# Performance work log

Measured on AMD Instinct MI355X. Metric: run time of the kernel, lower is better.

Reference implementation:

```python
import jax, jax.numpy as jnp
import numpy as np

B, L, D, H, K = 4, 2048, 1024, 16, 256
DH = D // H
SCALE = DH ** -0.5


def setup_inputs() -> dict:
    key = jax.random.key(0)
    ks = jax.random.split(key, 8)
    std = 1.0 / np.sqrt(D)
    pstd = 1.0 / np.sqrt(K)  # init_ uses last dim of (seq_len, k) tensor
    return {
        "x": jax.random.normal(ks[0], (B, L, D), dtype=jnp.float32),
        "Wq": jax.random.uniform(ks[1], (D, D), jnp.float32, -std, std),
        "Wk": jax.random.uniform(ks[2], (D, D), jnp.float32, -std, std),
        "Wv": jax.random.uniform(ks[3], (D, D), jnp.float32, -std, std),
        "proj_k": jax.random.uniform(ks[4], (L, K), jnp.float32, -pstd, pstd),
        "proj_v": jax.random.uniform(ks[5], (L, K), jnp.float32, -pstd, pstd),
        "Wo": jax.random.uniform(ks[6], (D, D), jnp.float32, -std, std),
        "bo": jax.random.uniform(ks[7], (D,), jnp.float32, -std, std),
    }


def reference(x, Wq, Wk, Wv, proj_k, proj_v, Wo, bo):
    b, l, d = x.shape
    q = x @ Wq.T                                   # [B,L,D]
    keys = jnp.einsum("bnd,nk->bkd", x @ Wk.T, proj_k)   # [B,K,D]
    vals = jnp.einsum("bnd,nk->bkd", x @ Wv.T, proj_v)   # [B,K,D]
    # faithful to original: plain reshape (B,h,L,d_h), NOT transpose-split
    q = q.reshape(b, H, l, DH)
    k = keys.reshape(b, K, H, DH).transpose(0, 2, 1, 3)  # [B,H,K,DH]
    v = vals.reshape(b, K, H, DH).transpose(0, 2, 1, 3)  # [B,H,K,DH]
    attn = jax.nn.softmax(jnp.einsum("bhld,bhkd->bhlk", q, k) * SCALE, axis=-1)
    out = jnp.einsum("bhlk,bhkd->bhld", attn, v)
    out = out.transpose(0, 2, 1, 3).reshape(b, l, d)
    return out @ Wo.T + bo
```

## Files before the change

kernel.cpp:

```cpp
#include <hip/hip_runtime.h>


typedef __attribute__((ext_vector_type(8))) short short8;
typedef __attribute__((ext_vector_type(4))) short short4_t;
typedef __attribute__((ext_vector_type(4))) float facc;

#define B_    4
#define L_    2048
#define D_    1024
#define H_    16
#define KP    256
#define DH_   64
#define SCALE_ 0.125f
#define PTS   76

__device__ __forceinline__ short f2b(float f) {
  unsigned u = __float_as_uint(f);
  unsigned r = (u + 0x7fffu + ((u >> 16) & 1u)) >> 16;
  return (short)r;
}

__device__ __forceinline__ void load16_to_lds(const short* gp, short* lp) {
  __builtin_amdgcn_global_load_lds(
      (const __attribute__((address_space(1))) void*)gp,
      (__attribute__((address_space(3))) void*)lp, 16, 0, 0);
}

__global__ __launch_bounds__(256) void prepX(
    const float* __restrict__ x,  const float* __restrict__ pk,
    const float* __restrict__ pv, const float* __restrict__ w0,
    const float* __restrict__ w1, const float* __restrict__ w2,
    const float* __restrict__ w3, short* __restrict__ xb,
    short* __restrict__ xTb, short* __restrict__ projT,
    short* __restrict__ Wb)
{
  const int z = blockIdx.z, tid = threadIdx.x;
  if (z >= 6) {
    const int bid  = blockIdx.y * 32 + blockIdx.x;
    const int widx = (z - 6) * 2 + (bid >> 10);
    const float* s = (widx == 0) ? w0 : (widx == 1) ? w1 : (widx == 2) ? w2 : w3;
    const int i = ((bid & 1023) * 256 + tid) * 4;
    float4 f = *(const float4*)(s + i);
    short4_t v; v[0] = f2b(f.x); v[1] = f2b(f.y); v[2] = f2b(f.z); v[3] = f2b(f.w);
    *(short4_t*)(Wb + (size_t)widx * 1048576 + i) = v;
    return;
  }

  __shared__ float tl[32][37];
  const int row = tid >> 3, c4 = tid & 7;

  if (z < 4) {
    const int b = z, l0 = blockIdx.y * 32, d0 = blockIdx.x * 32;
    const float* s = x + (size_t)b * L_ * D_;
    float4 f = *(const float4*)(s + (size_t)(l0 + row) * D_ + d0 + c4 * 4);
    short4_t v; v[0] = f2b(f.x); v[1] = f2b(f.y); v[2] = f2b(f.z); v[3] = f2b(f.w);
    *(short4_t*)(xb + (size_t)b * L_ * D_ + (size_t)(l0 + row) * D_ + d0 + c4 * 4) = v;
    tl[row][c4 * 4 + 0] = f.x; tl[row][c4 * 4 + 1] = f.y;
    tl[row][c4 * 4 + 2] = f.z; tl[row][c4 * 4 + 3] = f.w;
    __syncthreads();
    short4_t t;
#pragma unroll
    for (int j = 0; j < 4; j++) t[j] = f2b(tl[c4 * 4 + j][row]);
    *(short4_t*)(xTb + (size_t)b * D_ * L_ + (size_t)(d0 + row) * L_ + l0 + c4 * 4) = t;
  } else {
    if (blockIdx.x >= 8) return;
    const int sel = z - 4, l0 = blockIdx.y * 32, k0 = blockIdx.x * 32;
    const float* s = sel ? pv : pk;
    float4 f = *(const float4*)(s + (size_t)(l0 + row) * KP + k0 + c4 * 4);
    tl[row][c4 * 4 + 0] = f.x; tl[row][c4 * 4 + 1] = f.y;
    tl[row][c4 * 4 + 2] = f.z; tl[row][c4 * 4 + 3] = f.w;
    __syncthreads();
    short4_t t;
#pragma unroll
    for (int j = 0; j < 4; j++) t[j] = f2b(tl[c4 * 4 + j][row]);
    *(short4_t*)(projT + (size_t)sel * (KP * L_) + (size_t)(k0 + row) * L_ + l0 + c4 * 4) = t;
  }
}

__global__ __launch_bounds__(512, 2) void gemm8p(
    const short* __restrict__ Am, const short* __restrict__ Bm,
    const float* __restrict__ bias, float* __restrict__ C32,
    short* __restrict__ Cb, int M, int N, int K)
{
  extern __shared__ __attribute__((aligned(16))) short smem[];
  constexpr int BUF  = 24576;
  constexpr int BOFF = 16384;

  const int t = threadIdx.x, lane = t & 63, w = t >> 6;
  const int lm = lane & 15, g = lane >> 4;
  const int bm = blockIdx.x * 4 + (blockIdx.y >> 3);
  const int bn = blockIdx.y & 7;
  const int m0 = bm * 256, n0 = bn * 128;
  const int wm = (w & 3) * 64, wn = (w >> 2) * 64;

  const int srow = lane >> 2;
  const int sslot = lane & 3;

  facc acc[4][4];
  const facc fz = {0.f, 0.f, 0.f, 0.f};
#pragma unroll
  for (int i = 0; i < 4; i++)
#pragma unroll
    for (int j = 0; j < 4; j++) acc[i][j] = fz;

  auto stageA = [&](int kt, int buf, int rnd) {
    const int task = rnd * 8 + w;
    const int c = task >> 4, grp = task & 15;
    const int row = grp * 16 + srow;
    const int slot = sslot ^ ((row >> 1) & 3);
    load16_to_lds(Am + (size_t)(m0 + row) * K + kt * 64 + c * 32 + slot * 8,
                  smem + buf * BUF + c * 8192 + grp * 512);
  };
  auto stageB = [&](int kt, int buf, int rnd) {
    const int task = rnd * 8 + w;
    const int c = task >> 3, grp = task & 7;
    const int row = grp * 16 + srow;
    const int slot = sslot ^ ((row >> 1) & 3);
    load16_to_lds(Bm + (size_t)(n0 + row) * K + kt * 64 + c * 32 + slot * 8,
                  smem + buf * BUF + BOFF + c * 4096 + grp * 512);
  };

#pragma unroll
  for (int r = 0; r < 4; r++) stageA(0, 0, r);
#pragma unroll
  for (int r = 0; r < 2; r++) stageB(0, 0, r);
#pragma unroll
  for (int r = 0; r < 4; r++) stageA(1, 1, r);
#pragma unroll
  for (int r = 0; r < 2; r++) stageB(1, 1, r);
  asm volatile("s_waitcnt vmcnt(6)" ::: "memory");
  __builtin_amdgcn_sched_barrier(0);
  __builtin_amdgcn_s_barrier();

  const int T = K >> 6;
  int p = 0;
  for (int kt = 0; kt < T; kt++) {
    const int q = (p == 0) ? 2 : p - 1;
    const bool pf = (kt + 2 < T);

#pragma unroll
    for (int c = 0; c < 2; c++) {
      short8 af[4], bf[4];
      const int abase = p * BUF + c * 8192;
      const int bbase = p * BUF + BOFF + c * 4096;
#pragma unroll
      for (int mt = 0; mt < 4; mt++) {
        const int row = wm + 16 * mt + lm;
        af[mt] = *(const short8*)(smem + abase + row * 32 + ((g ^ ((row >> 1) & 3)) * 8));
      }
#pragma unroll
      for (int nt = 0; nt < 4; nt++) {
        const int row = wn + 16 * nt + lm;
        bf[nt] = *(const short8*)(smem + bbase + row * 32 + ((g ^ ((row >> 1) & 3)) * 8));
      }
      if (pf) {
        if (c == 0) { stageA(kt + 2, q, 0); stageA(kt + 2, q, 1); stageB(kt + 2, q, 0); }
        else        { stageA(kt + 2, q, 2); stageA(kt + 2, q, 3); stageB(kt + 2, q, 1); }
      }
      __builtin_amdgcn_s_barrier();
      __builtin_amdgcn_s_setprio(1);
#pragma unroll
      for (int mt = 0; mt < 4; mt++)
#pragma unroll
        for (int nt = 0; nt < 4; nt++)
          acc[mt][nt] = __builtin_amdgcn_mfma_f32_16x16x32_bf16(af[mt], bf[nt], acc[mt][nt], 0, 0, 0);
      __builtin_amdgcn_s_setprio(0);
      if (c == 0) __builtin_amdgcn_s_barrier();
    }

    if (pf) {
      asm volatile("s_waitcnt vmcnt(6)" ::: "memory");
      __builtin_amdgcn_sched_barrier(0);
    } else if (kt + 1 < T) {
      asm volatile("s_waitcnt vmcnt(0)" ::: "memory");
      __builtin_amdgcn_sched_barrier(0);
    }
    __builtin_amdgcn_s_barrier();
    p = (p == 2) ? 0 : p + 1;
  }

#pragma unroll
  for (int mt = 0; mt < 4; mt++)
#pragma unroll
    for (int r = 0; r < 4; r++) {
      const int row = m0 + wm + 16 * mt + 4 * g + r;
#pragma unroll
      for (int nt = 0; nt < 4; nt++) {
        const int col = n0 + wn + 16 * nt + lm;
        float v = acc[mt][nt][r];
        if (bias) v += bias[col];
        if (C32) C32[(size_t)row * N + col] = v;
        if (Cb)  Cb[(size_t)row * N + col] = f2b(v);
      }
    }
}

__global__ __launch_bounds__(256) void gemm_p64(
    const short* __restrict__ Am, const short* __restrict__ Bm,
    const float* __restrict__ bias, float* __restrict__ C32,
    short* __restrict__ Cb, short* __restrict__ CbT, int M, int N, int K,
    long aHi, long aLo, long bHi, long bLo, long cHi, long cLo, int zDiv)
{
  __shared__ __attribute__((aligned(16))) short smem[3 * 8192];
  const int t = threadIdx.x, lane = t & 63, w = t >> 6;
  const int lm = lane & 15, g = lane >> 4;
  const int z = blockIdx.z, zhi = z / zDiv, zlo = z % zDiv;
  const int bm = blockIdx.y, bn = blockIdx.x;
  const int m0 = bm * 64, n0 = bn * 64;
  const int wm = (w & 1) * 32, wn = (w >> 1) * 32;

  const short* Ab = Am + zhi * aHi + zlo * aLo;
  const short* Bp = Bm + zhi * bHi + zlo * bLo;

  const int srow = w * 16 + (lane >> 2);
  const int pslot = (lane & 3) ^ ((srow >> 1) & 3);

  facc acc[2][2];
  const facc fz = {0.f, 0.f, 0.f, 0.f};
#pragma unroll
  for (int i = 0; i < 2; i++)
#pragma unroll
    for (int j = 0; j < 2; j++) acc[i][j] = fz;

  auto stage_h = [&](int kt, int buf, int c) {
    load16_to_lds(Ab + (size_t)(m0 + srow) * K + kt * 64 + c * 32 + pslot * 8,
                  smem + buf * 8192 + c * 2048 + w * 512);
    load16_to_lds(Bp + (size_t)(n0 + srow) * K + kt * 64 + c * 32 + pslot * 8,
                  smem + buf * 8192 + 4096 + c * 2048 + w * 512);
  };

  stage_h(0, 0, 0); stage_h(0, 0, 1);
  stage_h(1, 1, 0); stage_h(1, 1, 1);
  asm volatile("s_waitcnt vmcnt(4)" ::: "memory");
  __builtin_amdgcn_sched_barrier(0);
  __builtin_amdgcn_s_barrier();

  const int T = K >> 6;
  int p = 0;
  for (int kt = 0; kt < T; kt++) {
    const int q = (p == 0) ? 2 : p - 1;
    const bool pf = (kt + 2 < T);

#pragma unroll
    for (int c = 0; c < 2; c++) {
      short8 af[2], bf[2];
      const int abase = p * 8192 + c * 2048;
      const int bbase = p * 8192 + 4096 + c * 2048;
#pragma unroll
      for (int mt = 0; mt < 2; mt++) {
        const int row = wm + 16 * mt + lm;
        af[mt] = *(const short8*)(smem + abase + row * 32 + ((g ^ ((row >> 1) & 3)) * 8));
      }
#pragma unroll
      for (int nt = 0; nt < 2; nt++) {
        const int row = wn + 16 * nt + lm;
        bf[nt] = *(const short8*)(smem + bbase + row * 32 + ((g ^ ((row >> 1) & 3)) * 8));
      }
      if (pf) stage_h(kt + 2, q, c);
      __builtin_amdgcn_s_setprio(1);
#pragma unroll
      for (int mt = 0; mt < 2; mt++)
#pragma unroll
        for (int nt = 0; nt < 2; nt++)
          acc[mt][nt] = __builtin_amdgcn_mfma_f32_16x16x32_bf16(af[mt], bf[nt], acc[mt][nt], 0, 0, 0);
      __builtin_amdgcn_s_setprio(0);
    }

    if (pf) {
      asm volatile("s_waitcnt vmcnt(4)" ::: "memory");
      __builtin_amdgcn_sched_barrier(0);
    } else if (kt + 1 < T) {
      asm volatile("s_waitcnt vmcnt(0)" ::: "memory");
      __builtin_amdgcn_sched_barrier(0);
    }
    __builtin_amdgcn_s_barrier();
    p = (p == 2) ? 0 : p + 1;
  }

  if (CbT && zhi == 1) {
#pragma unroll
    for (int mt = 0; mt < 2; mt++) {
      const int rb = m0 + wm + 16 * mt + 4 * g;
      const size_t bb = (size_t)(rb >> 8) * (16 * 64 * 256);
      const int kp = rb & 255;
#pragma unroll
      for (int nt = 0; nt < 2; nt++) {
        const int col = n0 + wn + 16 * nt + lm;
        short4_t o4;
#pragma unroll
        for (int r = 0; r < 4; r++) o4[r] = f2b(acc[mt][nt][r]);
        *(short4_t*)(CbT + bb + (size_t)col * KP + kp) = o4;
      }
    }
    return;
  }

  const long cz = zhi * cHi + zlo * cLo;
#pragma unroll
  for (int mt = 0; mt < 2; mt++)
#pragma unroll
    for (int r = 0; r < 4; r++) {
      const int row = m0 + wm + 16 * mt + 4 * g + r;
#pragma unroll
      for (int nt = 0; nt < 2; nt++) {
        const int col = n0 + wn + 16 * nt + lm;
        float v = acc[mt][nt][r];
        if (bias) v += bias[col];
        if (C32) C32[cz + (size_t)row * N + col] = v;
        if (Cb)  Cb[cz + (size_t)row * N + col] = f2b(v);
      }
    }
}

__global__ __launch_bounds__(256) void attn_mfma(
    const short* __restrict__ xqb, const short* __restrict__ keysb,
    const short* __restrict__ vTb, short* __restrict__ out2b)
{
  __shared__ __attribute__((aligned(16))) short Kt[2][64 * 72];
  __shared__ __attribute__((aligned(16))) short Vt[2][64 * 72];
  __shared__ __attribute__((aligned(16))) short Pt[4][32 * PTS];

  const int t = threadIdx.x, lane = t & 63, w = t >> 6;
  const int lm = lane & 15, g = lane >> 4;
  const int b = blockIdx.z, h = blockIdx.y;
  const int l0w = blockIdx.x * 128 + w * 32;

  short8 aq[2][2];
#pragma unroll
  for (int mt = 0; mt < 2; mt++) {
    const int l = l0w + 16 * mt + lm;
    const short* qrow = xqb + ((size_t)b * L_ + h * 128 + (l >> 4)) * D_ + (l & 15) * DH_;
#pragma unroll
    for (int ks = 0; ks < 2; ks++)
      aq[mt][ks] = *(const short8*)(qrow + ks * 32 + g * 8);
  }

  facc accO[2][4];
  const facc fz = {0.f, 0.f, 0.f, 0.f};
#pragma unroll
  for (int mt = 0; mt < 2; mt++)
#pragma unroll
    for (int dt = 0; dt < 4; dt++) accO[mt][dt] = fz;
  float lrow[2][4];
#pragma unroll
  for (int mt = 0; mt < 2; mt++)
#pragma unroll
    for (int r = 0; r < 4; r++) lrow[mt][r] = 0.f;

  const short* Kb = keysb + (size_t)b * KP * D_ + h * DH_;
  const short* Vb = vTb + ((size_t)b * H_ + h) * DH_ * KP;

  const int srow = t >> 3, sch = (t & 7) * 8;

#pragma unroll
  for (int i = 0; i < 2; i++) {
    const int row = srow + 32 * i;
    *(short8*)(&Kt[0][row * 72 + sch]) = *(const short8*)(Kb + (size_t)row * D_ + sch);
    *(short8*)(&Vt[0][row * 72 + sch]) = *(const short8*)(Vb + (size_t)row * KP + sch);
  }
  __syncthreads();

  for (int c = 0; c < 4; c++) {
    const int bi = c & 1;

    short8 kr[2], vr[2];
    if (c < 3) {
#pragma unroll
      for (int i = 0; i < 2; i++) {
        const int row = srow + 32 * i;
        kr[i] = *(const short8*)(Kb + (size_t)((c + 1) * 64 + row) * D_ + sch);
        vr[i] = *(const short8*)(Vb + (size_t)row * KP + (c + 1) * 64 + sch);
      }
    }

    facc S[2][4];
#pragma unroll
    for (int mt = 0; mt < 2; mt++)
#pragma unroll
      for (int nt = 0; nt < 4; nt++) S[mt][nt] = fz;
#pragma unroll
    for (int ks = 0; ks < 2; ks++) {
      short8 bk[4];
#pragma unroll
      for (int nt = 0; nt < 4; nt++)
        bk[nt] = *(const short8*)(&Kt[bi][(16 * nt + lm) * 72 + ks * 32 + g * 8]);
#pragma unroll
      for (int mt = 0; mt < 2; mt++)
#pragma unroll
        for (int nt = 0; nt < 4; nt++)
          S[mt][nt] = __builtin_amdgcn_mfma_f32_16x16x32_bf16(aq[mt][ks], bk[nt], S[mt][nt], 0, 0, 0);
    }

    if (c < 3) {
#pragma unroll
      for (int i = 0; i < 2; i++) {
        const int row = srow + 32 * i;
        *(short8*)(&Kt[bi ^ 1][row * 72 + sch]) = kr[i];
        *(short8*)(&Vt[bi ^ 1][row * 72 + sch]) = vr[i];
      }
    }

#pragma unroll
    for (int mt = 0; mt < 2; mt++)
#pragma unroll
      for (int r = 0; r < 4; r++) {
        float ps = 0.f;
        const int prow = (16 * mt + 4 * g + r) * PTS;
#pragma unroll
        for (int nt = 0; nt < 4; nt++) {
          const float p = __expf(S[mt][nt][r] * SCALE_);
          ps += p;
          Pt[w][prow + 16 * nt + lm] = f2b(p);
        }
        lrow[mt][r] += ps;
      }

#pragma unroll
    for (int ks = 0; ks < 2; ks++) {
      short8 ap[2], bv[4];
#pragma unroll
      for (int mt = 0; mt < 2; mt++)
        ap[mt] = *(const short8*)(&Pt[w][(16 * mt + lm) * PTS + ks * 32 + g * 8]);
#pragma unroll
      for (int dt = 0; dt < 4; dt++)
        bv[dt] = *(const short8*)(&Vt[bi][(16 * dt + lm) * 72 + ks * 32 + g * 8]);
#pragma unroll
      for (int mt = 0; mt < 2; mt++)
#pragma unroll
        for (int dt = 0; dt < 4; dt++)
          accO[mt][dt] = __builtin_amdgcn_mfma_f32_16x16x32_bf16(ap[mt], bv[dt], accO[mt][dt], 0, 0, 0);
    }
    __syncthreads();
  }

#pragma unroll
  for (int mt = 0; mt < 2; mt++)
#pragma unroll
    for (int r = 0; r < 4; r++) {
      float ls = lrow[mt][r];
      ls += __shfl_xor(ls, 1);
      ls += __shfl_xor(ls, 2);
      ls += __shfl_xor(ls, 4);
      ls += __shfl_xor(ls, 8);
      const float inv = 1.0f / ls;
      const int l = l0w + 16 * mt + 4 * g + r;
#pragma unroll
      for (int dt = 0; dt < 4; dt++)
        out2b[((size_t)b * L_ + l) * D_ + h * DH_ + 16 * dt + lm] = f2b(accO[mt][dt][r] * inv);
    }
}

extern "C" void kernel_launch(void* const* d_in, const int* in_sizes, int n_in,
                              void* d_out, int out_size, void* d_ws, size_t ws_size,
                              hipStream_t stream)
{
  const float* x      = (const float*)d_in[0];
  const float* Wq     = (const float*)d_in[1];
  const float* Wk     = (const float*)d_in[2];
  const float* Wv     = (const float*)d_in[3];
  const float* proj_k = (const float*)d_in[4];
  const float* proj_v = (const float*)d_in[5];
  const float* Wo     = (const float*)d_in[6];
  const float* bo     = (const float*)d_in[7];
  float* out = (float*)d_out;

  short* ws     = (short*)d_ws;
  short* xqb    = ws;
  short* xTb    = xqb    + 8388608;
  short* xb     = xTb    + 8388608;
  short* out2b  = xb;
  short* Wqb    = xb     + 8388608;
  short* Wkb    = Wqb    + 1048576;
  short* Wvb    = Wkb    + 1048576;
  short* Wob    = Wvb    + 1048576;
  short* projTk = Wob    + 1048576;
  short* projTv = projTk + 524288;
  short* xk2b   = projTv + 524288;
  short* xv2b   = xk2b   + 1048576;
  short* keysb  = xv2b   + 1048576;
  short* valsb  = keysb  + 1048576;
  short* vT     = valsb  + 1048576;
  (void)Wkb; (void)Wvb; (void)projTv; (void)xv2b; (void)valsb;

  static bool attr_set = false;
  if (!attr_set) {
    (void)hipFuncSetAttribute(reinterpret_cast<const void*>(gemm8p),
                              hipFuncAttributeMaxDynamicSharedMemorySize, 147456);
    attr_set = true;
  }

  prepX<<<dim3(32, 64, 8), 256, 0, stream>>>(
      x, proj_k, proj_v, Wq, Wk, Wv, Wo, xb, xTb, projTk, Wqb);

  gemm8p<<<dim3(8, 32, 1), 512, 147456, stream>>>(
      xb, Wqb, nullptr, nullptr, xqb, 8192, 1024, 1024);

  gemm_p64<<<dim3(16, 4, 8), 256, 0, stream>>>(
      projTk, xTb, nullptr, nullptr, xk2b, nullptr, 256, 1024, 2048,
      524288, 0, 0, (long)D_ * L_, 1048576, 262144, 4);

  gemm_p64<<<dim3(16, 16, 2), 256, 0, stream>>>(
      xk2b, Wkb, nullptr, nullptr, keysb, vT, 1024, 1024, 1024,
      1048576, 0, 1048576, 0, 0, 0, 1);

  attn_mfma<<<dim3(16, 16, 4), 256, 0, stream>>>(xqb, keysb, vT, out2b);

  gemm8p<<<dim3(8, 32, 1), 512, 147456, stream>>>(
      out2b, Wob, bo, out, nullptr, 8192, 1024, 1024);
}
```

Before: 216.0 us.

## Widen projection GEMM tile to 64x128 and read K/V directly in attention

The small projection GEMM kernel now computes a 64x128 output tile per block instead of 64x64. Each wave owns 32x64 of it, B staging loads double and the LDS ring grows, which is meant to raise MFMA work per A fetch and halve the grid. Separately, the attention kernel drops its double-buffered LDS staging of K and V and the per-chunk __syncthreads, and loads MFMA operands straight from global memory. That removes barriers and LDS traffic but relies on cache hits for repeated K/V reads across waves. The larger tile also halves the number of blocks, which may lower occupancy for these small GEMMs.

Result: slower. 234.6 us (+8.6%).

```diff
diff --git a/kernel.cpp b/kernel.cpp
--- a/kernel.cpp
+++ b/kernel.cpp
@@ -195,43 +195,50 @@
     }
 }
 
-__global__ __launch_bounds__(256) void gemm_p64(
+__global__ __launch_bounds__(256) void gemm_p64x128(
     const short* __restrict__ Am, const short* __restrict__ Bm,
     const float* __restrict__ bias, float* __restrict__ C32,
     short* __restrict__ Cb, short* __restrict__ CbT, int M, int N, int K,
     long aHi, long aLo, long bHi, long bLo, long cHi, long cLo, int zDiv)
 {
-  __shared__ __attribute__((aligned(16))) short smem[3 * 8192];
+  __shared__ __attribute__((aligned(16))) short smem[3 * 12288];
   const int t = threadIdx.x, lane = t & 63, w = t >> 6;
   const int lm = lane & 15, g = lane >> 4;
   const int z = blockIdx.z, zhi = z / zDiv, zlo = z % zDiv;
-  const int bm = blockIdx.y, bn = blockIdx.x;
-  const int m0 = bm * 64, n0 = bn * 64;
-  const int wm = (w & 1) * 32, wn = (w >> 1) * 32;
+  const int m0 = blockIdx.y * 64, n0 = blockIdx.x * 128;
+  const int wm = (w & 1) * 32, wn = (w >> 1) * 64;
 
   const short* Ab = Am + zhi * aHi + zlo * aLo;
   const short* Bp = Bm + zhi * bHi + zlo * bLo;
 
-  const int srow = w * 16 + (lane >> 2);
-  const int pslot = (lane & 3) ^ ((srow >> 1) & 3);
-
-  facc acc[2][2];
+  const int srow = lane >> 2;
+  const int sslot = lane & 3;
+
+  facc acc[2][4];
   const facc fz = {0.f, 0.f, 0.f, 0.f};
 #pragma unroll
   for (int i = 0; i < 2; i++)
 #pragma unroll
-    for (int j = 0; j < 2; j++) acc[i][j] = fz;
+    for (int j = 0; j < 4; j++) acc[i][j] = fz;
 
   auto stage_h = [&](int kt, int buf, int c) {
-    load16_to_lds(Ab + (size_t)(m0 + srow) * K + kt * 64 + c * 32 + pslot * 8,
-                  smem + buf * 8192 + c * 2048 + w * 512);
-    load16_to_lds(Bp + (size_t)(n0 + srow) * K + kt * 64 + c * 32 + pslot * 8,
-                  smem + buf * 8192 + 4096 + c * 2048 + w * 512);
+    const int arow = w * 16 + srow;
+    const int aslot = sslot ^ ((arow >> 1) & 3);
+    load16_to_lds(Ab + (size_t)(m0 + arow) * K + kt * 64 + c * 32 + aslot * 8,
+                  smem + buf * 12288 + c * 2048 + w * 512);
+#pragma unroll
+    for (int jj = 0; jj < 2; jj++) {
+      const int j = w + jj * 4;
+      const int brow = j * 16 + srow;
+      const int bslot = sslot ^ ((brow >> 1) & 3);
+      load16_to_lds(Bp + (size_t)(n0 + brow) * K + kt * 64 + c * 32 + bslot * 8,
+                    smem + buf * 12288 + 4096 + c * 4096 + j * 512);
+    }
   };
 
   stage_h(0, 0, 0); stage_h(0, 0, 1);
   stage_h(1, 1, 0); stage_h(1, 1, 1);
-  asm volatile("s_waitcnt vmcnt(4)" ::: "memory");
+  asm volatile("s_waitcnt vmcnt(6)" ::: "memory");
   __builtin_amdgcn_sched_barrier(0);
   __builtin_amdgcn_s_barrier();
 
@@ -243,16 +250,16 @@
 
 #pragma unroll
     for (int c = 0; c < 2; c++) {
-      short8 af[2], bf[2];
-      const int abase = p * 8192 + c * 2048;
-      const int bbase = p * 8192 + 4096 + c * 2048;
+      short8 af[2], bf[4];
+      const int abase = p * 12288 + c * 2048;
+      const int bbase = p * 12288 + 4096 + c * 4096;
 #pragma unroll
       for (int mt = 0; mt < 2; mt++) {
         const int row = wm + 16 * mt + lm;
         af[mt] = *(const short8*)(smem + abase + row * 32 + ((g ^ ((row >> 1) & 3)) * 8));
       }
 #pragma unroll
-      for (int nt = 0; nt < 2; nt++) {
+      for (int nt = 0; nt < 4; nt++) {
         const int row = wn + 16 * nt + lm;
         bf[nt] = *(const short8*)(smem + bbase + row * 32 + ((g ^ ((row >> 1) & 3)) * 8));
       }
@@ -261,13 +268,13 @@
 #pragma unroll
       for (int mt = 0; mt < 2; mt++)
 #pragma unroll
-        for (int nt = 0; nt < 2; nt++)
+        for (int nt = 0; nt < 4; nt++)
           acc[mt][nt] = __builtin_amdgcn_mfma_f32_16x16x32_bf16(af[mt], bf[nt], acc[mt][nt], 0, 0, 0);
       __builtin_amdgcn_s_setprio(0);
     }
 
     if (pf) {
-      asm volatile("s_waitcnt vmcnt(4)" ::: "memory");
+      asm volatile("s_waitcnt vmcnt(6)" ::: "memory");
       __builtin_amdgcn_sched_barrier(0);
     } else if (kt + 1 < T) {
       asm volatile("s_waitcnt vmcnt(0)" ::: "memory");
@@ -284,7 +291,7 @@
       const size_t bb = (size_t)(rb >> 8) * (16 * 64 * 256);
       const int kp = rb & 255;
 #pragma unroll
-      for (int nt = 0; nt < 2; nt++) {
+      for (int nt = 0; nt < 4; nt++) {
         const int col = n0 + wn + 16 * nt + lm;
         short4_t o4;
 #pragma unroll
@@ -302,7 +309,7 @@
     for (int r = 0; r < 4; r++) {
       const int row = m0 + wm + 16 * mt + 4 * g + r;
 #pragma unroll
-      for (int nt = 0; nt < 2; nt++) {
+      for (int nt = 0; nt < 4; nt++) {
         const int col = n0 + wn + 16 * nt + lm;
         float v = acc[mt][nt][r];
         if (bias) v += bias[col];
@@ -316,8 +323,6 @@
     const short* __restrict__ xqb, const short* __restrict__ keysb,
     const short* __restrict__ vTb, short* __restrict__ out2b)
 {
-  __shared__ __attribute__((aligned(16))) short Kt[2][64 * 72];
-  __shared__ __attribute__((aligned(16))) short Vt[2][64 * 72];
   __shared__ __attribute__((aligned(16))) short Pt[4][32 * PTS];
 
   const int t = threadIdx.x, lane = t & 63, w = t >> 6;
@@ -350,29 +355,7 @@
   const short* Kb = keysb + (size_t)b * KP * D_ + h * DH_;
   const short* Vb = vTb + ((size_t)b * H_ + h) * DH_ * KP;
 
-  const int srow = t >> 3, sch = (t & 7) * 8;
-
-#pragma unroll
-  for (int i = 0; i < 2; i++) {
-    const int row = srow + 32 * i;
-    *(short8*)(&Kt[0][row * 72 + sch]) = *(const short8*)(Kb + (size_t)row * D_ + sch);
-    *(short8*)(&Vt[0][row * 72 + sch]) = *(const short8*)(Vb + (size_t)row * KP + sch);
-  }
-  __syncthreads();
-
   for (int c = 0; c < 4; c++) {
-    const int bi = c & 1;
-
-    short8 kr[2], vr[2];
-    if (c < 3) {
-#pragma unroll
-      for (int i = 0; i < 2; i++) {
-        const int row = srow + 32 * i;
-        kr[i] = *(const short8*)(Kb + (size_t)((c + 1) * 64 + row) * D_ + sch);
-        vr[i] = *(const short8*)(Vb + (size_t)row * KP + (c + 1) * 64 + sch);
-      }
-    }
-
     facc S[2][4];
 #pragma unroll
     for (int mt = 0; mt < 2; mt++)
@@ -383,21 +366,12 @@
       short8 bk[4];
 #pragma unroll
       for (int nt = 0; nt < 4; nt++)
-        bk[nt] = *(const short8*)(&Kt[bi][(16 * nt + lm) * 72 + ks * 32 + g * 8]);
+        bk[nt] = *(const short8*)(Kb + (size_t)(c * 64 + 16 * nt + lm) * D_ + ks * 32 + g * 8);
 #pragma unroll
       for (int mt = 0; mt < 2; mt++)
 #pragma unroll
         for (int nt = 0; nt < 4; nt++)
           S[mt][nt] = __builtin_amdgcn_mfma_f32_16x16x32_bf16(aq[mt][ks], bk[nt], S[mt][nt], 0, 0, 0);
-    }
-
-    if (c < 3) {
-#pragma unroll
-      for (int i = 0; i < 2; i++) {
-        const int row = srow + 32 * i;
-        *(short8*)(&Kt[bi ^ 1][row * 72 + sch]) = kr[i];
-        *(short8*)(&Vt[bi ^ 1][row * 72 + sch]) = vr[i];
-      }
     }
 
 #pragma unroll
@@ -423,14 +397,13 @@
         ap[mt] = *(const short8*)(&Pt[w][(16 * mt + lm) * PTS + ks * 32 + g * 8]);
 #pragma unroll
       for (int dt = 0; dt < 4; dt++)
-        bv[dt] = *(const short8*)(&Vt[bi][(16 * dt + lm) * 72 + ks * 32 + g * 8]);
+        bv[dt] = *(const short8*)(Vb + (size_t)(16 * dt + lm) * KP + c * 64 + ks * 32 + g * 8);
 #pragma unroll
       for (int mt = 0; mt < 2; mt++)
 #pragma unroll
         for (int dt = 0; dt < 4; dt++)
           accO[mt][dt] = __builtin_amdgcn_mfma_f32_16x16x32_bf16(ap[mt], bv[dt], accO[mt][dt], 0, 0, 0);
     }
-    __syncthreads();
   }
 
 #pragma unroll
@@ -495,11 +468,11 @@
   gemm8p<<<dim3(8, 32, 1), 512, 147456, stream>>>(
       xb, Wqb, nullptr, nullptr, xqb, 8192, 1024, 1024);
 
-  gemm_p64<<<dim3(16, 4, 8), 256, 0, stream>>>(
+  gemm_p64x128<<<dim3(8, 4, 8), 256, 0, stream>>>(
       projTk, xTb, nullptr, nullptr, xk2b, nullptr, 256, 1024, 2048,
       524288, 0, 0, (long)D_ * L_, 1048576, 262144, 4);
 
-  gemm_p64<<<dim3(16, 16, 2), 256, 0, stream>>>(
+  gemm_p64x128<<<dim3(8, 16, 2), 256, 0, stream>>>(
       xk2b, Wkb, nullptr, nullptr, keysb, vT, 1024, 1024, 1024,
       1048576, 0, 1048576, 0, 0, 0, 1);
 
```
